# Kernel tuning notes

Hardware: AMD Instinct MI355X
Metric: run time of the kernel (lower is better)

Reference implementation:

```python
import jax, jax.numpy as jnp
import numpy as np

IN_FT = 256
OUT_FT = 256


def setup_inputs() -> dict:
    key = jax.random.key(0)
    k1, k2, k3 = jax.random.split(key, 3)
    B, N = 4, 4096
    seq = jax.random.normal(k1, (B, N, IN_FT), dtype=jnp.float32)
    adj = jax.random.uniform(k2, (B, N, N), dtype=jnp.float32)
    # Xavier-uniform fc weight [out_ft, in_ft], bias zeros
    limit = float(np.sqrt(6.0 / (IN_FT + OUT_FT)))
    W = jax.random.uniform(k3, (OUT_FT, IN_FT), minval=-limit, maxval=limit, dtype=jnp.float32)
    b = jnp.zeros((OUT_FT,), dtype=jnp.float32)
    alpha = jnp.array(0.25, dtype=jnp.float32)  # PReLU shared parameter
    return {"seq": seq, "adj": adj, "W": W, "b": b, "alpha": alpha}


def reference(seq, adj, W, b, alpha):
    # Linear projection: [B, N, out_ft]
    h = jnp.einsum("bni,oi->bno", seq, W) + b
    # Neighbor aggregation (dense bmm path): [B, N, N] @ [B, N, out_ft]
    h = jnp.einsum("bnm,bmo->bno", adj, h)
    # PReLU with shared alpha
    return jnp.where(h > 0, h, alpha * h)
```

## Files before the change

### kernel.cpp

```cpp
#include <hip/hip_runtime.h>
#include <hip/hip_bf16.h>

#define NSEQ 4096
#define FT 256
#define BK 64
#define BKB 128
#define NTB (NSEQ / BKB)

typedef __attribute__((ext_vector_type(8))) short bf16x8;
typedef __attribute__((ext_vector_type(4))) float f32x4;

__device__ __forceinline__ ushort f2bf(float f) {
  __hip_bfloat16 h = __float2bfloat16(f);
  return *reinterpret_cast<const ushort*>(&h);
}

__device__ __forceinline__ int swz(int row, int byteInRow) {
  return row * 128 + (byteInRow ^ ((row & 7) << 4));
}

__device__ __forceinline__ void mma_step(const char* lAp, const char* lBp,
                                         int lane, int wm, int wn,
                                         f32x4 acc[2][4]) {
  const int r16 = lane & 15;
  const int g16 = (lane >> 4) * 16;
#pragma unroll
  for (int kk = 0; kk < 2; ++kk) {
    const int kb = kk * 64 + g16;
    bf16x8 a[2], b[4];
#pragma unroll
    for (int mi = 0; mi < 2; ++mi) {
      const int row = wm * 32 + mi * 16 + r16;
      a[mi] = *reinterpret_cast<const bf16x8*>(lAp + swz(row, kb));
    }
#pragma unroll
    for (int ni = 0; ni < 4; ++ni) {
      const int row = wn * 64 + ni * 16 + r16;
      b[ni] = *reinterpret_cast<const bf16x8*>(lBp + swz(row, kb));
    }
#pragma unroll
    for (int mi = 0; mi < 2; ++mi)
#pragma unroll
      for (int ni = 0; ni < 4; ++ni)
        acc[mi][ni] = __builtin_amdgcn_mfma_f32_16x16x32_bf16(a[mi], b[ni],
                                                             acc[mi][ni], 0, 0, 0);
  }
}

__global__ __launch_bounds__(512) void linear_kernel(
    const float* __restrict__ seq, const float* __restrict__ W,
    const float* __restrict__ bias, ushort* __restrict__ hT) {
  __shared__ __align__(16) ushort lA[2][64 * 64];
  __shared__ __align__(16) ushort lB[2][256 * 64];

  const int tid = threadIdx.x;
  const int lane = tid & 63;
  const int wid = tid >> 6;
  const int wm = wid >> 2, wn = wid & 3;
  const int m0 = blockIdx.x * 64;

  const int ar = tid >> 4, ac = tid & 15;

  f32x4 rA[2];
  f32x4 rB[8];

  auto gload = [&](int t) {
    const int k0 = t * BK;
#pragma unroll
    for (int p = 0; p < 2; ++p)
      rA[p] = *reinterpret_cast<const f32x4*>(
          seq + (size_t)(m0 + ar + p * 32) * FT + k0 + ac * 4);
#pragma unroll
    for (int p = 0; p < 8; ++p)
      rB[p] = *reinterpret_cast<const f32x4*>(
          W + (size_t)(ar + p * 32) * FT + k0 + ac * 4);
  };
  auto lwrite = [&](int buf) {
    char* lAp = (char*)lA[buf];
    char* lBp = (char*)lB[buf];
#pragma unroll
    for (int p = 0; p < 2; ++p) {
      ushort4 u = make_ushort4(f2bf(rA[p][0]), f2bf(rA[p][1]), f2bf(rA[p][2]), f2bf(rA[p][3]));
      *reinterpret_cast<ushort4*>(lAp + swz(ar + p * 32, ac * 8)) = u;
    }
#pragma unroll
    for (int p = 0; p < 8; ++p) {
      ushort4 u = make_ushort4(f2bf(rB[p][0]), f2bf(rB[p][1]), f2bf(rB[p][2]), f2bf(rB[p][3]));
      *reinterpret_cast<ushort4*>(lBp + swz(ar + p * 32, ac * 8)) = u;
    }
  };

  f32x4 acc[2][4];
  const f32x4 zero = {0.f, 0.f, 0.f, 0.f};
#pragma unroll
  for (int mi = 0; mi < 2; ++mi)
#pragma unroll
    for (int ni = 0; ni < 4; ++ni) acc[mi][ni] = zero;

  gload(0);
  lwrite(0);
  const int NTA = FT / BK;
  for (int t = 0; t < NTA; ++t) {
    const int cur = t & 1;
    __syncthreads();
    if (t + 1 < NTA) gload(t + 1);
    mma_step((const char*)lA[cur], (const char*)lB[cur], lane, wm, wn, acc);
    if (t + 1 < NTA) lwrite(cur ^ 1);
  }

  __syncthreads();
  ushort* lT = (ushort*)&lB[0][0];
  const int TP = 72;
#pragma unroll
  for (int mi = 0; mi < 2; ++mi) {
    const int rbase = wm * 32 + mi * 16 + ((lane >> 4) << 2);
#pragma unroll
    for (int ni = 0; ni < 4; ++ni) {
      const int o = wn * 64 + ni * 16 + (lane & 15);
      const float bo = bias[o];
      ushort4 u;
      u.x = f2bf(acc[mi][ni][0] + bo);
      u.y = f2bf(acc[mi][ni][1] + bo);
      u.z = f2bf(acc[mi][ni][2] + bo);
      u.w = f2bf(acc[mi][ni][3] + bo);
      *reinterpret_cast<ushort4*>(&lT[o * TP + rbase]) = u;
    }
  }
  __syncthreads();
  const int batch = (blockIdx.x * 64) >> 12;
  const int n0 = (blockIdx.x * 64) & (NSEQ - 1);
  const int o = tid >> 1, hf = tid & 1;
  ushort* dst = hT + ((size_t)(batch * FT + o)) * NSEQ + n0 + hf * 32;
#pragma unroll
  for (int k = 0; k < 4; ++k) {
    uint4 v = *reinterpret_cast<const uint4*>(&lT[o * TP + hf * 32 + k * 8]);
    *reinterpret_cast<uint4*>(dst + k * 8) = v;
  }
}

__global__ __launch_bounds__(512) void bmm_prelu_kernel(
    const float* __restrict__ adj, const ushort* __restrict__ hT,
    const float* __restrict__ alphaP, float* __restrict__ out) {
  __shared__ __align__(16) char smem[2 * 65536 + 2 * 16384];

  const int tid = threadIdx.x;
  const int lane = tid & 63;
  const int wid = tid >> 6;
  const int wm = wid >> 2, wn = wid & 3;

  const int bid = blockIdx.x;
  const int sbid = (bid & 7) * 32 + (bid >> 3);
  const int batch = sbid >> 6;
  const int m0 = (sbid & 63) * 64;

  const float* adjB = adj + (size_t)batch * NSEQ * NSEQ + (size_t)m0 * NSEQ;
  const ushort* hTB = hT + (size_t)batch * FT * NSEQ;

  auto lB = [&](int i) -> char* { return smem + i * 65536; };
  auto lA = [&](int i) -> char* { return smem + 131072 + i * 16384; };

  const int arow = tid >> 3, ac = tid & 7;
  const int bro = (lane >> 4);
  const int bhalf = (lane >> 3) & 1;
  f32x4 rS[4];

  f32x4 acc[2][4];
  const f32x4 zero = {0.f, 0.f, 0.f, 0.f};
#pragma unroll
  for (int mi = 0; mi < 2; ++mi)
#pragma unroll
    for (int ni = 0; ni < 4; ++ni) acc[mi][ni] = zero;

  auto issueA = [&](int t) {
    const int k0 = t * BKB;
#pragma unroll
    for (int q = 0; q < 4; ++q)
      rS[q] = *reinterpret_cast<const f32x4*>(
          adjB + (size_t)arow * NSEQ + k0 + ac * 16 + q * 4);
  };
  auto issueB = [&](int t, int ib) {
    const int k0 = t * BKB;
#pragma unroll
    for (int p = 0; p < 8; ++p) {
      const int grow = wid * 32 + p * 4 + bro;
      const int gsrc = (lane & 7) ^ (((p & 1) * 4 + bro) & 7);
      const ushort* gp = hTB + (size_t)grow * NSEQ + k0 + bhalf * 64 + gsrc * 8;
      char* lp = lB(ib) + wid * 8192 + p * 1024;
      __builtin_amdgcn_global_load_lds(
          (const __attribute__((address_space(1))) void*)gp,
          (__attribute__((address_space(3))) void*)lp, 16, 0, 0);
    }
  };
  auto writeA = [&](int ia) {
    char* lAp = lA(ia);
    const int half = ac >> 2;
#pragma unroll
    for (int q = 0; q < 4; ++q) {
      ushort4 u = make_ushort4(f2bf(rS[q][0]), f2bf(rS[q][1]),
                               f2bf(rS[q][2]), f2bf(rS[q][3]));
      const int gih = (((ac & 3) * 2 + (q >> 1)) ^ (arow & 7));
      *reinterpret_cast<ushort4*>(lAp + arow * 256 + half * 128 + gih * 16 +
                                  (q & 1) * 8) = u;
    }
  };
  auto mma32 = [&](const char* lAp, const char* lBp) {
    const int r16 = lane & 15;
    const int sub = lane >> 4;
#pragma unroll
    for (int kk = 0; kk < 4; ++kk) {
      const int half = kk >> 1;
      const int gih = (((kk & 1) * 4 + sub) ^ (r16 & 7));
      const int bofs = half * 128 + gih * 16;
      bf16x8 a[2], b[4];
#pragma unroll
      for (int mi = 0; mi < 2; ++mi) {
        const int row = wm * 32 + mi * 16 + r16;
        a[mi] = *reinterpret_cast<const bf16x8*>(lAp + row * 256 + bofs);
      }
#pragma unroll
      for (int ni = 0; ni < 4; ++ni) {
        const int row = wn * 64 + ni * 16 + r16;
        b[ni] = *reinterpret_cast<const bf16x8*>(lBp + row * 256 + bofs);
      }
#pragma unroll
      for (int mi = 0; mi < 2; ++mi)
#pragma unroll
        for (int ni = 0; ni < 4; ++ni)
          acc[mi][ni] = __builtin_amdgcn_mfma_f32_16x16x32_bf16(
              a[mi], b[ni], acc[mi][ni], 0, 0, 0);
    }
  };

  issueA(0);
  __builtin_amdgcn_sched_barrier(0);
  issueB(0, 0);
  __builtin_amdgcn_sched_barrier(0);
  asm volatile("s_waitcnt vmcnt(8)" ::: "memory");
  __builtin_amdgcn_sched_barrier(0);
  writeA(0);
  asm volatile("s_waitcnt vmcnt(0) lgkmcnt(0)" ::: "memory");
  __builtin_amdgcn_s_barrier();
  __builtin_amdgcn_sched_barrier(0);

  auto body = [&](int t, int cur) {
    issueA(t + 1);
    __builtin_amdgcn_sched_barrier(0);
    issueB(t + 1, cur ^ 1);
    __builtin_amdgcn_sched_barrier(0);
    __builtin_amdgcn_s_setprio(1);
    mma32(lA(cur), lB(cur));
    __builtin_amdgcn_s_setprio(0);
    asm volatile("s_waitcnt vmcnt(8)" ::: "memory");
    __builtin_amdgcn_sched_barrier(0);
    writeA(cur ^ 1);
    asm volatile("s_waitcnt vmcnt(0) lgkmcnt(0)" ::: "memory");
    __builtin_amdgcn_s_barrier();
    __builtin_amdgcn_sched_barrier(0);
  };

  for (int j = 0; j < 15; ++j) {
    body(2 * j, 0);
    body(2 * j + 1, 1);
  }
  body(30, 0);
  __builtin_amdgcn_s_setprio(1);
  mma32(lA(1), lB(1));
  __builtin_amdgcn_s_setprio(0);

  const float alpha = *alphaP;
  __syncthreads();
  float* lo = (float*)smem;
  const int PITCH = 264;
#pragma unroll
  for (int mi = 0; mi < 2; ++mi) {
    const int rbase = wm * 32 + mi * 16 + ((lane >> 4) << 2);
#pragma unroll
    for (int ni = 0; ni < 4; ++ni) {
      const int o = wn * 64 + ni * 16 + (lane & 15);
#pragma unroll
      for (int j = 0; j < 4; ++j) {
        float v = acc[mi][ni][j];
        v = v > 0.f ? v : alpha * v;
        lo[(rbase + j) * PITCH + o] = v;
      }
    }
  }
  __syncthreads();
  float* outB = out + ((size_t)batch * NSEQ + m0) * FT;
  const int r = tid >> 3, c8 = tid & 7;
#pragma unroll
  for (int k = 0; k < 8; ++k) {
    const int g = c8 + k * 8;
    f32x4 v = *reinterpret_cast<const f32x4*>(lo + r * PITCH + g * 4);
    __builtin_nontemporal_store(v, reinterpret_cast<f32x4*>(outB + (size_t)r * FT + g * 4));
  }
}

extern "C" void kernel_launch(void* const* d_in, const int* in_sizes, int n_in,
                              void* d_out, int out_size, void* d_ws, size_t ws_size,
                              hipStream_t stream) {
  const float* seq = (const float*)d_in[0];
  const float* adj = (const float*)d_in[1];
  const float* W = (const float*)d_in[2];
  const float* bias = (const float*)d_in[3];
  const float* alpha = (const float*)d_in[4];
  float* out = (float*)d_out;
  ushort* hT = (ushort*)d_ws;

  linear_kernel<<<256, 512, 0, stream>>>(seq, W, bias, hT);
  bmm_prelu_kernel<<<256, 512, 0, stream>>>(adj, hT, alpha, out);
}
```

Measured before the change: 83.72 us.

## Reassociate to (adj@seq)@W^T, fusing linear projection into bmm epilogue

Replaces the separate linear GEMM kernel with a cheap transpose-and-cast of seq, then computes adj@seq in the main kernel and applies W in the epilogue via a second small MFMA GEMM. The bias term is handled by accumulating adj row sums during A staging and adding bias*rowsum. This removes the linear kernel's GEMM ahead of the big bmm, at the cost of an extra epilogue GEMM per block and an extra bf16 rounding of the intermediate adj@seq result.

```diff
diff --git a/kernel.cpp b/kernel.cpp
--- a/kernel.cpp
+++ b/kernel.cpp
@@ -3,9 +3,7 @@
 
 #define NSEQ 4096
 #define FT 256
-#define BK 64
 #define BKB 128
-#define NTB (NSEQ / BKB)
 
 typedef __attribute__((ext_vector_type(8))) short bf16x8;
 typedef __attribute__((ext_vector_type(4))) float f32x4;
@@ -19,134 +17,43 @@
   return row * 128 + (byteInRow ^ ((row & 7) << 4));
 }
 
-__device__ __forceinline__ void mma_step(const char* lAp, const char* lBp,
-                                         int lane, int wm, int wn,
-                                         f32x4 acc[2][4]) {
-  const int r16 = lane & 15;
-  const int g16 = (lane >> 4) * 16;
-#pragma unroll
-  for (int kk = 0; kk < 2; ++kk) {
-    const int kb = kk * 64 + g16;
-    bf16x8 a[2], b[4];
-#pragma unroll
-    for (int mi = 0; mi < 2; ++mi) {
-      const int row = wm * 32 + mi * 16 + r16;
-      a[mi] = *reinterpret_cast<const bf16x8*>(lAp + swz(row, kb));
-    }
-#pragma unroll
-    for (int ni = 0; ni < 4; ++ni) {
-      const int row = wn * 64 + ni * 16 + r16;
-      b[ni] = *reinterpret_cast<const bf16x8*>(lBp + swz(row, kb));
-    }
-#pragma unroll
-    for (int mi = 0; mi < 2; ++mi)
-#pragma unroll
-      for (int ni = 0; ni < 4; ++ni)
-        acc[mi][ni] = __builtin_amdgcn_mfma_f32_16x16x32_bf16(a[mi], b[ni],
-                                                             acc[mi][ni], 0, 0, 0);
-  }
-}
-
-__global__ __launch_bounds__(512) void linear_kernel(
-    const float* __restrict__ seq, const float* __restrict__ W,
-    const float* __restrict__ bias, ushort* __restrict__ hT) {
-  __shared__ __align__(16) ushort lA[2][64 * 64];
-  __shared__ __align__(16) ushort lB[2][256 * 64];
+__global__ __launch_bounds__(512) void transpose_cast_kernel(
+    const float* __restrict__ seq, ushort* __restrict__ seqT) {
+  __shared__ __align__(16) ushort lT[256 * 72];
+
+  const int tid = threadIdx.x;
+  const int batch = blockIdx.x >> 6;
+  const int n0 = (blockIdx.x & 63) * 64;
+  const float* src = seq + ((size_t)batch * NSEQ + n0) * FT;
+
+  const int ar = tid >> 3, ac = tid & 7;
+#pragma unroll
+  for (int p = 0; p < 8; ++p) {
+    const int fb = (ac + p * 8) * 4;
+    f32x4 v = *reinterpret_cast<const f32x4*>(src + (size_t)ar * FT + fb);
+#pragma unroll
+    for (int e = 0; e < 4; ++e) lT[(fb + e) * 72 + ar] = f2bf(v[e]);
+  }
+  __syncthreads();
+  const int f = tid >> 1, hf = tid & 1;
+  ushort* dst = seqT + ((size_t)(batch * FT + f)) * NSEQ + n0 + hf * 32;
+#pragma unroll
+  for (int k = 0; k < 4; ++k) {
+    uint4 v = *reinterpret_cast<const uint4*>(&lT[f * 72 + hf * 32 + k * 8]);
+    *reinterpret_cast<uint4*>(dst + k * 8) = v;
+  }
+}
+
+__global__ __launch_bounds__(512) void bmm_prelu_kernel(
+    const float* __restrict__ adj, const ushort* __restrict__ seqT,
+    const float* __restrict__ W, const float* __restrict__ bias,
+    const float* __restrict__ alphaP, float* __restrict__ out) {
+  __shared__ __align__(16) char smem[2 * 65536 + 2 * 16384];
 
   const int tid = threadIdx.x;
   const int lane = tid & 63;
   const int wid = tid >> 6;
   const int wm = wid >> 2, wn = wid & 3;
-  const int m0 = blockIdx.x * 64;
-
-  const int ar = tid >> 4, ac = tid & 15;
-
-  f32x4 rA[2];
-  f32x4 rB[8];
-
-  auto gload = [&](int t) {
-    const int k0 = t * BK;
-#pragma unroll
-    for (int p = 0; p < 2; ++p)
-      rA[p] = *reinterpret_cast<const f32x4*>(
-          seq + (size_t)(m0 + ar + p * 32) * FT + k0 + ac * 4);
-#pragma unroll
-    for (int p = 0; p < 8; ++p)
-      rB[p] = *reinterpret_cast<const f32x4*>(
-          W + (size_t)(ar + p * 32) * FT + k0 + ac * 4);
-  };
-  auto lwrite = [&](int buf) {
-    char* lAp = (char*)lA[buf];
-    char* lBp = (char*)lB[buf];
-#pragma unroll
-    for (int p = 0; p < 2; ++p) {
-      ushort4 u = make_ushort4(f2bf(rA[p][0]), f2bf(rA[p][1]), f2bf(rA[p][2]), f2bf(rA[p][3]));
-      *reinterpret_cast<ushort4*>(lAp + swz(ar + p * 32, ac * 8)) = u;
-    }
-#pragma unroll
-    for (int p = 0; p < 8; ++p) {
-      ushort4 u = make_ushort4(f2bf(rB[p][0]), f2bf(rB[p][1]), f2bf(rB[p][2]), f2bf(rB[p][3]));
-      *reinterpret_cast<ushort4*>(lBp + swz(ar + p * 32, ac * 8)) = u;
-    }
-  };
-
-  f32x4 acc[2][4];
-  const f32x4 zero = {0.f, 0.f, 0.f, 0.f};
-#pragma unroll
-  for (int mi = 0; mi < 2; ++mi)
-#pragma unroll
-    for (int ni = 0; ni < 4; ++ni) acc[mi][ni] = zero;
-
-  gload(0);
-  lwrite(0);
-  const int NTA = FT / BK;
-  for (int t = 0; t < NTA; ++t) {
-    const int cur = t & 1;
-    __syncthreads();
-    if (t + 1 < NTA) gload(t + 1);
-    mma_step((const char*)lA[cur], (const char*)lB[cur], lane, wm, wn, acc);
-    if (t + 1 < NTA) lwrite(cur ^ 1);
-  }
-
-  __syncthreads();
-  ushort* lT = (ushort*)&lB[0][0];
-  const int TP = 72;
-#pragma unroll
-  for (int mi = 0; mi < 2; ++mi) {
-    const int rbase = wm * 32 + mi * 16 + ((lane >> 4) << 2);
-#pragma unroll
-    for (int ni = 0; ni < 4; ++ni) {
-      const int o = wn * 64 + ni * 16 + (lane & 15);
-      const float bo = bias[o];
-      ushort4 u;
-      u.x = f2bf(acc[mi][ni][0] + bo);
-      u.y = f2bf(acc[mi][ni][1] + bo);
-      u.z = f2bf(acc[mi][ni][2] + bo);
-      u.w = f2bf(acc[mi][ni][3] + bo);
-      *reinterpret_cast<ushort4*>(&lT[o * TP + rbase]) = u;
-    }
-  }
-  __syncthreads();
-  const int batch = (blockIdx.x * 64) >> 12;
-  const int n0 = (blockIdx.x * 64) & (NSEQ - 1);
-  const int o = tid >> 1, hf = tid & 1;
-  ushort* dst = hT + ((size_t)(batch * FT + o)) * NSEQ + n0 + hf * 32;
-#pragma unroll
-  for (int k = 0; k < 4; ++k) {
-    uint4 v = *reinterpret_cast<const uint4*>(&lT[o * TP + hf * 32 + k * 8]);
-    *reinterpret_cast<uint4*>(dst + k * 8) = v;
-  }
-}
-
-__global__ __launch_bounds__(512) void bmm_prelu_kernel(
-    const float* __restrict__ adj, const ushort* __restrict__ hT,
-    const float* __restrict__ alphaP, float* __restrict__ out) {
-  __shared__ __align__(16) char smem[2 * 65536 + 2 * 16384];
-
-  const int tid = threadIdx.x;
-  const int lane = tid & 63;
-  const int wid = tid >> 6;
-  const int wm = wid >> 2, wn = wid & 3;
 
   const int bid = blockIdx.x;
   const int sbid = (bid & 7) * 32 + (bid >> 3);
@@ -154,7 +61,7 @@
   const int m0 = (sbid & 63) * 64;
 
   const float* adjB = adj + (size_t)batch * NSEQ * NSEQ + (size_t)m0 * NSEQ;
-  const ushort* hTB = hT + (size_t)batch * FT * NSEQ;
+  const ushort* hTB = seqT + (size_t)batch * FT * NSEQ;
 
   auto lB = [&](int i) -> char* { return smem + i * 65536; };
   auto lA = [&](int i) -> char* { return smem + 131072 + i * 16384; };
@@ -163,6 +70,7 @@
   const int bro = (lane >> 4);
   const int bhalf = (lane >> 3) & 1;
   f32x4 rS[4];
+  float rsum = 0.f;
 
   f32x4 acc[2][4];
   const f32x4 zero = {0.f, 0.f, 0.f, 0.f};
@@ -196,6 +104,7 @@
     const int half = ac >> 2;
 #pragma unroll
     for (int q = 0; q < 4; ++q) {
+      rsum += rS[q][0] + rS[q][1] + rS[q][2] + rS[q][3];
       ushort4 u = make_ushort4(f2bf(rS[q][0]), f2bf(rS[q][1]),
                                f2bf(rS[q][2]), f2bf(rS[q][3]));
       const int gih = (((ac & 3) * 2 + (q >> 1)) ^ (arow & 7));
@@ -269,6 +178,78 @@
 
   const float alpha = *alphaP;
   __syncthreads();
+
+  ushort* lT64 = (ushort*)smem;
+  float* rsP = (float*)(smem + 98304);
+  float* rsW = (float*)(smem + 100352);
+  const int TP2 = 264;
+#pragma unroll
+  for (int mi = 0; mi < 2; ++mi) {
+    const int rbase = wm * 32 + mi * 16 + ((lane >> 4) << 2);
+#pragma unroll
+    for (int ni = 0; ni < 4; ++ni) {
+      const int f = wn * 64 + ni * 16 + (lane & 15);
+#pragma unroll
+      for (int j = 0; j < 4; ++j) lT64[(rbase + j) * TP2 + f] = f2bf(acc[mi][ni][j]);
+    }
+  }
+  rsP[arow * 8 + ac] = rsum;
+  __syncthreads();
+  if (tid < 64) {
+    float s = 0.f;
+#pragma unroll
+    for (int i = 0; i < 8; ++i) s += rsP[tid * 8 + i];
+    rsW[tid] = s;
+  }
+
+  ushort* lW = (ushort*)(smem + 49152);
+  f32x4 accO[2][4];
+#pragma unroll
+  for (int mi = 0; mi < 2; ++mi)
+#pragma unroll
+    for (int ni = 0; ni < 4; ++ni) accO[mi][ni] = zero;
+  const int war = tid >> 4, wac = tid & 15;
+  for (int c = 0; c < 4; ++c) {
+    __syncthreads();
+    f32x4 rW[8];
+#pragma unroll
+    for (int p = 0; p < 8; ++p)
+      rW[p] = *reinterpret_cast<const f32x4*>(
+          W + (size_t)(war + p * 32) * FT + c * 64 + wac * 4);
+#pragma unroll
+    for (int p = 0; p < 8; ++p) {
+      ushort4 u = make_ushort4(f2bf(rW[p][0]), f2bf(rW[p][1]),
+                               f2bf(rW[p][2]), f2bf(rW[p][3]));
+      *reinterpret_cast<ushort4*>((char*)lW + swz(war + p * 32, wac * 8)) = u;
+    }
+    __syncthreads();
+    const int r16 = lane & 15;
+    const int g16 = (lane >> 4) * 16;
+#pragma unroll
+    for (int kk = 0; kk < 2; ++kk) {
+      const int kb = kk * 64 + g16;
+      const int fo = c * 64 + kk * 32 + (lane >> 4) * 8;
+      bf16x8 a[2], b[4];
+#pragma unroll
+      for (int mi = 0; mi < 2; ++mi) {
+        const int row = wm * 32 + mi * 16 + r16;
+        a[mi] = *reinterpret_cast<const bf16x8*>(&lT64[row * TP2 + fo]);
+      }
+#pragma unroll
+      for (int ni = 0; ni < 4; ++ni) {
+        const int row = wn * 64 + ni * 16 + r16;
+        b[ni] = *reinterpret_cast<const bf16x8*>((char*)lW + swz(row, kb));
+      }
+#pragma unroll
+      for (int mi = 0; mi < 2; ++mi)
+#pragma unroll
+        for (int ni = 0; ni < 4; ++ni)
+          accO[mi][ni] = __builtin_amdgcn_mfma_f32_16x16x32_bf16(
+              a[mi], b[ni], accO[mi][ni], 0, 0, 0);
+    }
+  }
+
+  __syncthreads();
   float* lo = (float*)smem;
   const int PITCH = 264;
 #pragma unroll
@@ -277,9 +258,10 @@
 #pragma unroll
     for (int ni = 0; ni < 4; ++ni) {
       const int o = wn * 64 + ni * 16 + (lane & 15);
+      const float bo = bias[o];
 #pragma unroll
       for (int j = 0; j < 4; ++j) {
-        float v = acc[mi][ni][j];
+        float v = accO[mi][ni][j] + bo * rsW[rbase + j];
         v = v > 0.f ? v : alpha * v;
         lo[(rbase + j) * PITCH + o] = v;
       }
@@ -305,8 +287,8 @@
   const float* bias = (const float*)d_in[3];
   const float* alpha = (const float*)d_in[4];
   float* out = (float*)d_out;
-  ushort* hT = (ushort*)d_ws;
-
-  linear_kernel<<<256, 512, 0, stream>>>(seq, W, bias, hT);
-  bmm_prelu_kernel<<<256, 512, 0, stream>>>(adj, hT, alpha, out);
-}
+  ushort* seqT = (ushort*)d_ws;
+
+  transpose_cast_kernel<<<256, 512, 0, stream>>>(seq, seqT);
+  bmm_prelu_kernel<<<256, 512, 0, stream>>>(adj, seqT, W, bias, alpha, out);
+}
```

Measured after the change: 83.34 us. No clear change (-0.4%).
